# Kernel tuning notes

Hardware: AMD Instinct MI355X
Metric: run time of the kernel (lower is better)

Reference implementation:

```python
import jax, jax.numpy as jnp
import numpy as np
from jax import lax

B, CM, CQ, CO, H, W, KS = 8, 64, 64, 64, 128, 128, 3
K = KS * KS  # 9 kernel taps, offset_group=1


def setup_inputs() -> dict:
    key = jax.random.key(0)
    k1, k2, k3, k4 = jax.random.split(key, 4)
    mem = jax.random.normal(k1, (B, CM, H, W), jnp.float32)
    que = jax.random.normal(k2, (B, CQ, H, W), jnp.float32)
    # conv_offset: Conv2d(CM+CQ -> 3*K, 3x3, pad=1, bias=True); small init so offsets are a few px
    w_off = jax.random.normal(k3, (3 * K, CM + CQ, KS, KS), jnp.float32) * 0.01
    b_off = jnp.zeros((3 * K,), jnp.float32)
    # deformable conv weight: [CO, CM, 3, 3], bias=False
    w_def = jax.random.normal(k4, (CO, CM, KS, KS), jnp.float32) * (1.0 / np.sqrt(CM * K))
    return {"mem": mem, "que": que, "w_off": w_off, "b_off": b_off, "w_def": w_def}


def _deform_conv2d(mem, offset, mask, w_def):
    """Deformable conv v2 (stride=1, pad=1, dil=1, groups=1, offset_group=1).
    mem: [B,C,H,W]; offset: [B,2K,H,W] (dy,dx pairs per tap); mask: [B,K,H,W]."""
    Bn, C, Hn, Wn = mem.shape
    Kn = w_def.shape[2] * w_def.shape[3]
    off = offset.reshape(Bn, Kn, 2, Hn, Wn)
    dy, dx = off[:, :, 0], off[:, :, 1]            # [B,K,H,W]
    kk = jnp.arange(Kn)
    ky = (kk // KS - 1).astype(jnp.float32)        # kernel tap offsets with pad=1, dil=1
    kx = (kk % KS - 1).astype(jnp.float32)
    gy = jnp.arange(Hn, dtype=jnp.float32)
    gx = jnp.arange(Wn, dtype=jnp.float32)
    py = gy[None, None, :, None] + ky[None, :, None, None] + dy   # sample y coords [B,K,H,W]
    px = gx[None, None, None, :] + kx[None, :, None, None] + dx   # sample x coords [B,K,H,W]
    y0 = jnp.floor(py)
    x0 = jnp.floor(px)
    fy = py - y0
    fx = px - x0
    b_idx = jnp.arange(Bn)[:, None, None, None]

    def corner(iy, ix, wgt):
        valid = (iy >= 0) & (iy < Hn) & (ix >= 0) & (ix < Wn)  # zero padding outside
        iyc = jnp.clip(iy.astype(jnp.int32), 0, Hn - 1)
        ixc = jnp.clip(ix.astype(jnp.int32), 0, Wn - 1)
        vals = mem[b_idx, :, iyc, ixc]             # gather -> [B,K,H,W,C]
        return vals * (wgt * valid)[..., None]

    sampled = (corner(y0, x0, (1 - fy) * (1 - fx))
               + corner(y0, x0 + 1, (1 - fy) * fx)
               + corner(y0 + 1, x0, fy * (1 - fx))
               + corner(y0 + 1, x0 + 1, fy * fx))
    sampled = sampled * mask[..., None]            # modulation (applied raw, as in source)
    w = w_def.reshape(w_def.shape[0], C, Kn)       # [O,C,K]; tap order kh*KS+kw matches kk
    return jnp.einsum('bkhwc,ock->bohw', sampled, w)


def reference(mem, que, w_off, b_off, w_def):
    x = jnp.concatenate([mem, que], axis=1)
    off = lax.conv_general_dilated(
        x, w_off, window_strides=(1, 1), padding=[(1, 1), (1, 1)],
        dimension_numbers=('NCHW', 'OIHW', 'NCHW')) + b_off[None, :, None, None]
    offset, mask = off[:, :2 * K], off[:, 2 * K:]
    return _deform_conv2d(mem, offset, mask, w_def)
```

## Files before the change

kernel.cpp:

```cpp
#include <hip/hip_runtime.h>
#include <hip/hip_fp16.h>

#define Bn   8
#define CM_  64
#define CIN  128
#define CO_  64
#define Hn   128
#define Wn   128
#define Kn   9
#define COFF 27
#define HW   (Hn * Wn)

typedef __attribute__((ext_vector_type(8))) _Float16 f16x8;
typedef __attribute__((ext_vector_type(4))) float f32x4;

__device__ __forceinline__ unsigned h22u(__half2 h) {
    unsigned u; __builtin_memcpy(&u, &h, 4); return u;
}
__device__ __forceinline__ __half2 u2h2(unsigned u) {
    __half2 h; __builtin_memcpy(&h, &u, 4); return h;
}
__device__ __forceinline__ unsigned short f2h(float x) {
    __half h = __float2half(x);
    unsigned short u; __builtin_memcpy(&u, &h, 2); return u;
}

__global__ __launch_bounds__(256) void transpose_kernel(
    const float* __restrict__ mem, const float* __restrict__ que,
    uint4* __restrict__ xT4)
{
    __shared__ unsigned tile[64 * 65];

    const int bb   = blockIdx.x & 7;
    const int pix0 = (blockIdx.x >> 3) * 64;
    const int tid  = threadIdx.x;
    const int pxL  = tid & 63;
    const int cg   = tid >> 6;

    const float* mb = mem + (size_t)bb * CM_ * HW + pix0 + pxL;
    const float* qb = que + (size_t)bb * CM_ * HW + pix0 + pxL;

    #pragma unroll
    for (int i = 0; i < 16; ++i) {
        const int c = cg * 32 + 2 * i;
        const float v0 = (c < CM_) ? mb[(size_t)c * HW]       : qb[(size_t)(c - CM_) * HW];
        const float v1 = (c + 1 < CM_) ? mb[(size_t)(c + 1) * HW] : qb[(size_t)(c + 1 - CM_) * HW];
        tile[pxL * 65 + cg * 16 + i] = h22u(__floats2half2_rn(v0, v1));
    }
    __syncthreads();

    uint4* dst = xT4 + (size_t)(bb * HW + pix0) * 16;
    #pragma unroll
    for (int p = 0; p < 4; ++p) {
        const int G  = p * 256 + tid;
        const int px = G >> 4;
        const int u  = G & 15;
        uint4 v;
        v.x = tile[px * 65 + u * 4 + 0];
        v.y = tile[px * 65 + u * 4 + 1];
        v.z = tile[px * 65 + u * 4 + 2];
        v.w = tile[px * 65 + u * 4 + 3];
        dst[G] = v;
    }
}

__global__ __launch_bounds__(256) void wprep_all_kernel(
    const float* __restrict__ w_def, const float* __restrict__ w_off,
    unsigned short* __restrict__ wpd, unsigned short* __restrict__ wpo)
{
    int idx = blockIdx.x * 256 + threadIdx.x;
    if (idx < CO_ * CM_ * Kn) {
        const int j  = idx & 7;
        const int L  = (idx >> 3) & 63;
        const int f  = (idx >> 9) & 1;
        const int gk = idx >> 10;
        const int k  = gk % 9;
        const int g  = gk / 9;
        const int o  = g * 16 + (L & 15);
        const int c  = f * 32 + (L >> 4) * 8 + j;
        wpd[idx] = f2h(w_def[(size_t)(o * CM_ + c) * Kn + k]);
        return;
    }
    idx -= CO_ * CM_ * Kn;
    if (idx < 2 * 9 * 4 * 64 * 8) {
        const int j   = idx & 7;
        const int L   = (idx >> 3) & 63;
        const int s   = (idx >> 9) & 3;
        const int r   = idx >> 11;
        const int tap = r % 9;
        const int ot  = r / 9;
        const int o   = ot * 16 + (L & 15);
        const int c   = s * 32 + (L >> 4) * 8 + j;
        wpo[idx] = (o < COFF) ? f2h(w_off[(size_t)(o * CIN + c) * Kn + tap])
                              : (unsigned short)0;
    }
}

__global__ __launch_bounds__(256, 6) void fused_deform_kernel(
    const uint4* __restrict__ xT4, const uint4* __restrict__ wpo,
    const uint4* __restrict__ wpd, const float* __restrict__ b_off,
    float* __restrict__ out)
{
    __shared__ __align__(16) char lds[198 * 8 * 16];
    uint4* xw   = (uint4*)lds;
    float* offl = (float*)lds;
    uint4* smp4 = (uint4*)(lds + 8192);

    const int bb   = blockIdx.x & 7;
    const int pix0 = (blockIdx.x >> 3) * 64;
    const int h0   = pix0 >> 7;
    const int w0   = pix0 & 127;
    const int tid  = threadIdx.x;
    const int wv   = tid >> 6;
    const int lane = tid & 63;
    const int quad = lane >> 4;
    const int lrow = lane & 15;

    const uint4* xb = xT4 + (size_t)bb * HW * 16;

    {
        const int ot   = wv >> 1;
        const int sub0 = (wv & 1) * 2;

        f32x4 oacc[2];
        #pragma unroll
        for (int t = 0; t < 2; ++t)
            #pragma unroll
            for (int r = 0; r < 4; ++r) {
                const int o = ot * 16 + quad * 4 + r;
                oacc[t][r] = (o < COFF) ? b_off[o] : 0.0f;
            }

        #pragma unroll
        for (int Hh = 0; Hh < 2; ++Hh) {
            #pragma unroll
            for (int g = 0; g < 7; ++g) {
                const int idx = g * 256 + tid;
                if (idx < 198 * 8) {
                    const int slot = idx >> 3;
                    const int j    = idx & 7;
                    const int r    = slot / 66;
                    const int c    = slot - r * 66;
                    const int y    = h0 + r - 1;
                    const int x    = w0 + c - 1;
                    const bool ok  = (y >= 0) & (y < Hn) & (x >= 0) & (x < Wn);
                    uint4 v = make_uint4(0, 0, 0, 0);
                    if (ok) v = xb[(size_t)(y * Wn + x) * 16 + Hh * 8 + j];
                    xw[slot * 8 + (j ^ (slot & 7))] = v;
                }
            }
            __syncthreads();

            #pragma unroll
            for (int tap = 0; tap < 9; ++tap) {
                const int rr = tap / 3;
                const int cc = tap % 3;

                const uint4* ap = wpo
                    + (size_t)((ot * 9 + tap) * 4 + Hh * 2) * 64 + lane;
                f16x8 a[2];
                #pragma unroll
                for (int s = 0; s < 2; ++s)
                    a[s] = __builtin_bit_cast(f16x8, ap[s * 64]);

                #pragma unroll
                for (int t = 0; t < 2; ++t) {
                    const int pl   = (sub0 + t) * 16 + lrow;
                    const int slot = rr * 66 + pl + cc;
                    const int base = slot * 8;
                    const int sw   = slot & 7;
                    #pragma unroll
                    for (int s = 0; s < 2; ++s) {
                        const f16x8 bfrag = __builtin_bit_cast(f16x8,
                            xw[base + ((s * 4 + quad) ^ sw)]);
                        oacc[t] = __builtin_amdgcn_mfma_f32_16x16x32_f16(
                            a[s], bfrag, oacc[t], 0, 0, 0);
                    }
                }
            }
            __syncthreads();
        }

        #pragma unroll
        for (int t = 0; t < 2; ++t) {
            const int pl = (sub0 + t) * 16 + lrow;
            #pragma unroll
            for (int r = 0; r < 4; ++r) {
                const int o = ot * 16 + quad * 4 + r;
                if (o < COFF) offl[o * 64 + pl] = oacc[t][r];
            }
        }
        __syncthreads();
    }

    const int chunk = lane & 7;
    const int psub  = lane >> 3;

    const int pM = pix0 + lane;
    const int hM = pM >> 7;
    const int wM = pM & 127;

    f32x4 acc[4];
    #pragma unroll
    for (int i = 0; i < 4; ++i) acc[i] = (f32x4){0.f, 0.f, 0.f, 0.f};

    __half2 W00h[2], W01h[2], W10h[2], W11h[2];
    uint4   G00[2], G01[2], G10[2], G11[2];

    auto prep = [&](int k) {
        const float dy = offl[(2 * k    ) * 64 + lane];
        const float dx = offl[(2 * k + 1) * 64 + lane];
        const float mk = offl[(18 + k   ) * 64 + lane];
        const float py = (float)(hM + k / 3 - 1) + dy;
        const float px = (float)(wM + k % 3 - 1) + dx;
        const float y0f = floorf(py), x0f = floorf(px);
        const float fy = py - y0f,  fx = px - x0f;
        const int y0 = (int)y0f, x0 = (int)x0f;
        const int y1 = y0 + 1,   x1 = x0 + 1;
        const bool vy0 = (y0 >= 0) & (y0 < Hn);
        const bool vy1 = (y1 >= 0) & (y1 < Hn);
        const bool vx0 = (x0 >= 0) & (x0 < Wn);
        const bool vx1 = (x1 >= 0) & (x1 < Wn);
        const float w00 = (1.f - fy) * (1.f - fx) * (float)(vy0 & vx0) * mk;
        const float w01 = (1.f - fy) * fx         * (float)(vy0 & vx1) * mk;
        const float w10 = fy * (1.f - fx)         * (float)(vy1 & vx0) * mk;
        const float w11 = fy * fx                 * (float)(vy1 & vx1) * mk;
        const int y0c = min(max(y0, 0), Hn - 1);
        const int y1c = min(max(y1, 0), Hn - 1);
        const int x0c = min(max(x0, 0), Wn - 1);
        const int x1c = min(max(x1, 0), Wn - 1);
        const int i00 = y0c * Wn + x0c, i01 = y0c * Wn + x1c;
        const int i10 = y1c * Wn + x0c, i11 = y1c * Wn + x1c;

        #pragma unroll
        for (int g = 0; g < 2; ++g) {
            const int pl = g * 32 + wv * 8 + psub;
            W00h[g] = __float2half2_rn(__shfl(w00, pl, 64));
            W01h[g] = __float2half2_rn(__shfl(w01, pl, 64));
            W10h[g] = __float2half2_rn(__shfl(w10, pl, 64));
            W11h[g] = __float2half2_rn(__shfl(w11, pl, 64));
            const int I00 = __shfl(i00, pl, 64);
            const int I01 = __shfl(i01, pl, 64);
            const int I10 = __shfl(i10, pl, 64);
            const int I11 = __shfl(i11, pl, 64);
            G00[g] = xb[(size_t)I00 * 16 + chunk];
            G01[g] = xb[(size_t)I01 * 16 + chunk];
            G10[g] = xb[(size_t)I10 * 16 + chunk];
            G11[g] = xb[(size_t)I11 * 16 + chunk];
        }
    };

    auto blendwrite = [&](int buf) {
        #pragma unroll
        for (int g = 0; g < 2; ++g) {
            const int pl = g * 32 + wv * 8 + psub;
            const unsigned u00[4] = {G00[g].x, G00[g].y, G00[g].z, G00[g].w};
            const unsigned u01[4] = {G01[g].x, G01[g].y, G01[g].z, G01[g].w};
            const unsigned u10[4] = {G10[g].x, G10[g].y, G10[g].z, G10[g].w};
            const unsigned u11[4] = {G11[g].x, G11[g].y, G11[g].z, G11[g].w};
            unsigned pk[4];
            #pragma unroll
            for (int d = 0; d < 4; ++d) {
                __half2 s = __hmul2(u2h2(u00[d]), W00h[g]);
                s = __hfma2(u2h2(u01[d]), W01h[g], s);
                s = __hfma2(u2h2(u10[d]), W10h[g], s);
                s = __hfma2(u2h2(u11[d]), W11h[g], s);
                pk[d] = h22u(s);
            }
            smp4[buf * 512 + pl * 8 + (chunk ^ (pl & 7))] =
                make_uint4(pk[0], pk[1], pk[2], pk[3]);
        }
    };

    prep(0);
    blendwrite(0);
    __syncthreads();

    #pragma unroll
    for (int k = 0; k < Kn; ++k) {
        const int cur = k & 1;

        if (k < Kn - 1) prep(k + 1);

        const uint4* wpk = wpd + (size_t)((wv * 9 + k) * 2) * 64 + lane;
        const f16x8 a0 = __builtin_bit_cast(f16x8, wpk[0]);
        const f16x8 a1 = __builtin_bit_cast(f16x8, wpk[64]);

        #pragma unroll
        for (int nt = 0; nt < 4; ++nt) {
            const int pm = nt * 16 + lrow;
            const f16x8 b0 = __builtin_bit_cast(f16x8,
                smp4[cur * 512 + pm * 8 + ( quad      ^ (pm & 7))]);
            const f16x8 b1 = __builtin_bit_cast(f16x8,
                smp4[cur * 512 + pm * 8 + ((quad + 4) ^ (pm & 7))]);
            acc[nt] = __builtin_amdgcn_mfma_f32_16x16x32_f16(a0, b0, acc[nt], 0, 0, 0);
            acc[nt] = __builtin_amdgcn_mfma_f32_16x16x32_f16(a1, b1, acc[nt], 0, 0, 0);
        }

        if (k < Kn - 1) blendwrite(cur ^ 1);
        __syncthreads();
    }

    const int obase = (wv << 4) + (quad << 2);
    #pragma unroll
    for (int nt = 0; nt < 4; ++nt) {
        const int pp = pix0 + nt * 16 + lrow;
        #pragma unroll
        for (int r = 0; r < 4; ++r)
            out[(size_t)(bb * CO_ + obase + r) * HW + pp] = acc[nt][r];
    }
}

extern "C" void kernel_launch(void* const* d_in, const int* in_sizes, int n_in,
                              void* d_out, int out_size, void* d_ws, size_t ws_size,
                              hipStream_t stream) {
    const float* mem   = (const float*)d_in[0];
    const float* que   = (const float*)d_in[1];
    const float* w_off = (const float*)d_in[2];
    const float* b_off = (const float*)d_in[3];
    const float* w_def = (const float*)d_in[4];
    float* out = (float*)d_out;

    char* ws = (char*)d_ws;
    unsigned short* wpd = (unsigned short*)ws;
    unsigned short* wpo = (unsigned short*)(ws + 73728);
    uint4*          xT4 = (uint4*)(ws + 147456);

    transpose_kernel<<<2048, 256, 0, stream>>>(mem, que, xT4);
    wprep_all_kernel<<<288, 256, 0, stream>>>(w_def, w_off, wpd, wpo);
    fused_deform_kernel<<<2048, 256, 0, stream>>>(
        xT4, (const uint4*)wpo, (const uint4*)wpd, b_off, out);
}
```

Baseline: 180.3 us.

## Make deformable-conv phase wave-local to remove per-tap block barriers

Restructures the sampling/GEMM phase so each wave owns 16 pixels and computes all 64 output channels for them, instead of each wave owning 16 output channels across all 64 pixels. Each lane now computes its own bilinear weights and gathers, with no cross-lane shuffles. The sampled tile lives in a per-wave LDS region, which removes the per-tap __syncthreads. The weight-prep layout is reordered to match, the LDS layout is rearranged, one barrier in the offset-conv loop is skipped, and the occupancy hint in launch_bounds is dropped. In exchange, each wave loads all of the deform weights from global/cache every tap, and the per-wave LDS buffer relies on wave-synchronous ordering without an explicit barrier.

```diff
diff --git a/kernel.cpp b/kernel.cpp
--- a/kernel.cpp
+++ b/kernel.cpp
@@ -73,9 +73,9 @@
         const int j  = idx & 7;
         const int L  = (idx >> 3) & 63;
         const int f  = (idx >> 9) & 1;
-        const int gk = idx >> 10;
-        const int k  = gk % 9;
-        const int g  = gk / 9;
+        const int q  = idx >> 10;
+        const int k  = q >> 2;
+        const int g  = q & 3;
         const int o  = g * 16 + (L & 15);
         const int c  = f * 32 + (L >> 4) * 8 + j;
         wpd[idx] = f2h(w_def[(size_t)(o * CM_ + c) * Kn + k]);
@@ -96,15 +96,14 @@
     }
 }
 
-__global__ __launch_bounds__(256, 6) void fused_deform_kernel(
+__global__ __launch_bounds__(256) void fused_deform_kernel(
     const uint4* __restrict__ xT4, const uint4* __restrict__ wpo,
     const uint4* __restrict__ wpd, const float* __restrict__ b_off,
     float* __restrict__ out)
 {
-    __shared__ __align__(16) char lds[198 * 8 * 16];
+    __shared__ __align__(16) char lds[32256];
     uint4* xw   = (uint4*)lds;
-    float* offl = (float*)lds;
-    uint4* smp4 = (uint4*)(lds + 8192);
+    float* offl = (float*)(lds + 25344);
 
     const int bb   = blockIdx.x & 7;
     const int pix0 = (blockIdx.x >> 3) * 64;
@@ -178,7 +177,7 @@
                     }
                 }
             }
-            __syncthreads();
+            if (Hh == 0) __syncthreads();
         }
 
         #pragma unroll
@@ -193,28 +192,30 @@
         __syncthreads();
     }
 
-    const int chunk = lane & 7;
-    const int psub  = lane >> 3;
-
-    const int pM = pix0 + lane;
+    const int px = lane & 15;
+    const int cs = lane >> 4;
+    const int sp = wv * 16 + px;
+    const int pM = pix0 + sp;
     const int hM = pM >> 7;
     const int wM = pM & 127;
 
+    uint4* smpW = (uint4*)lds + wv * 256;
+
     f32x4 acc[4];
     #pragma unroll
     for (int i = 0; i < 4; ++i) acc[i] = (f32x4){0.f, 0.f, 0.f, 0.f};
 
-    __half2 W00h[2], W01h[2], W10h[2], W11h[2];
-    uint4   G00[2], G01[2], G10[2], G11[2];
+    __half2 Wc00, Wc01, Wc10, Wc11;
+    uint4 G[8];
 
     auto prep = [&](int k) {
-        const float dy = offl[(2 * k    ) * 64 + lane];
-        const float dx = offl[(2 * k + 1) * 64 + lane];
-        const float mk = offl[(18 + k   ) * 64 + lane];
-        const float py = (float)(hM + k / 3 - 1) + dy;
-        const float px = (float)(wM + k % 3 - 1) + dx;
-        const float y0f = floorf(py), x0f = floorf(px);
-        const float fy = py - y0f,  fx = px - x0f;
+        const float dy = offl[(2 * k    ) * 64 + sp];
+        const float dx = offl[(2 * k + 1) * 64 + sp];
+        const float mk = offl[(18 + k   ) * 64 + sp];
+        const float py  = (float)(hM + k / 3 - 1) + dy;
+        const float pxf = (float)(wM + k % 3 - 1) + dx;
+        const float y0f = floorf(py), x0f = floorf(pxf);
+        const float fy = py - y0f,  fx = pxf - x0f;
         const int y0 = (int)y0f, x0 = (int)x0f;
         const int y1 = y0 + 1,   x1 = x0 + 1;
         const bool vy0 = (y0 >= 0) & (y0 < Hn);
@@ -225,89 +226,76 @@
         const float w01 = (1.f - fy) * fx         * (float)(vy0 & vx1) * mk;
         const float w10 = fy * (1.f - fx)         * (float)(vy1 & vx0) * mk;
         const float w11 = fy * fx                 * (float)(vy1 & vx1) * mk;
+        Wc00 = __float2half2_rn(w00);
+        Wc01 = __float2half2_rn(w01);
+        Wc10 = __float2half2_rn(w10);
+        Wc11 = __float2half2_rn(w11);
         const int y0c = min(max(y0, 0), Hn - 1);
         const int y1c = min(max(y1, 0), Hn - 1);
         const int x0c = min(max(x0, 0), Wn - 1);
         const int x1c = min(max(x1, 0), Wn - 1);
         const int i00 = y0c * Wn + x0c, i01 = y0c * Wn + x1c;
         const int i10 = y1c * Wn + x0c, i11 = y1c * Wn + x1c;
-
-        #pragma unroll
-        for (int g = 0; g < 2; ++g) {
-            const int pl = g * 32 + wv * 8 + psub;
-            W00h[g] = __float2half2_rn(__shfl(w00, pl, 64));
-            W01h[g] = __float2half2_rn(__shfl(w01, pl, 64));
-            W10h[g] = __float2half2_rn(__shfl(w10, pl, 64));
-            W11h[g] = __float2half2_rn(__shfl(w11, pl, 64));
-            const int I00 = __shfl(i00, pl, 64);
-            const int I01 = __shfl(i01, pl, 64);
-            const int I10 = __shfl(i10, pl, 64);
-            const int I11 = __shfl(i11, pl, 64);
-            G00[g] = xb[(size_t)I00 * 16 + chunk];
-            G01[g] = xb[(size_t)I01 * 16 + chunk];
-            G10[g] = xb[(size_t)I10 * 16 + chunk];
-            G11[g] = xb[(size_t)I11 * 16 + chunk];
-        }
+        const uint4* p00 = xb + (size_t)i00 * 16 + cs;
+        const uint4* p01 = xb + (size_t)i01 * 16 + cs;
+        const uint4* p10 = xb + (size_t)i10 * 16 + cs;
+        const uint4* p11 = xb + (size_t)i11 * 16 + cs;
+        G[0] = p00[0]; G[1] = p00[4];
+        G[2] = p01[0]; G[3] = p01[4];
+        G[4] = p10[0]; G[5] = p10[4];
+        G[6] = p11[0]; G[7] = p11[4];
     };
 
-    auto blendwrite = [&](int buf) {
-        #pragma unroll
-        for (int g = 0; g < 2; ++g) {
-            const int pl = g * 32 + wv * 8 + psub;
-            const unsigned u00[4] = {G00[g].x, G00[g].y, G00[g].z, G00[g].w};
-            const unsigned u01[4] = {G01[g].x, G01[g].y, G01[g].z, G01[g].w};
-            const unsigned u10[4] = {G10[g].x, G10[g].y, G10[g].z, G10[g].w};
-            const unsigned u11[4] = {G11[g].x, G11[g].y, G11[g].z, G11[g].w};
+    auto blend_store = [&](int buf) {
+        #pragma unroll
+        for (int hh = 0; hh < 2; ++hh) {
+            const uint4 g00 = G[0 + hh], g01 = G[2 + hh];
+            const uint4 g10 = G[4 + hh], g11 = G[6 + hh];
+            const unsigned u00[4] = {g00.x, g00.y, g00.z, g00.w};
+            const unsigned u01[4] = {g01.x, g01.y, g01.z, g01.w};
+            const unsigned u10[4] = {g10.x, g10.y, g10.z, g10.w};
+            const unsigned u11[4] = {g11.x, g11.y, g11.z, g11.w};
             unsigned pk[4];
             #pragma unroll
             for (int d = 0; d < 4; ++d) {
-                __half2 s = __hmul2(u2h2(u00[d]), W00h[g]);
-                s = __hfma2(u2h2(u01[d]), W01h[g], s);
-                s = __hfma2(u2h2(u10[d]), W10h[g], s);
-                s = __hfma2(u2h2(u11[d]), W11h[g], s);
+                __half2 s = __hmul2(u2h2(u00[d]), Wc00);
+                s = __hfma2(u2h2(u01[d]), Wc01, s);
+                s = __hfma2(u2h2(u10[d]), Wc10, s);
+                s = __hfma2(u2h2(u11[d]), Wc11, s);
                 pk[d] = h22u(s);
             }
-            smp4[buf * 512 + pl * 8 + (chunk ^ (pl & 7))] =
+            smpW[buf * 128 + px * 8 + ((cs + hh * 4) ^ (px & 7))] =
                 make_uint4(pk[0], pk[1], pk[2], pk[3]);
         }
     };
 
     prep(0);
-    blendwrite(0);
-    __syncthreads();
-
     #pragma unroll
     for (int k = 0; k < Kn; ++k) {
-        const int cur = k & 1;
-
+        const int buf = k & 1;
+        blend_store(buf);
         if (k < Kn - 1) prep(k + 1);
 
-        const uint4* wpk = wpd + (size_t)((wv * 9 + k) * 2) * 64 + lane;
-        const f16x8 a0 = __builtin_bit_cast(f16x8, wpk[0]);
-        const f16x8 a1 = __builtin_bit_cast(f16x8, wpk[64]);
-
-        #pragma unroll
-        for (int nt = 0; nt < 4; ++nt) {
-            const int pm = nt * 16 + lrow;
-            const f16x8 b0 = __builtin_bit_cast(f16x8,
-                smp4[cur * 512 + pm * 8 + ( quad      ^ (pm & 7))]);
-            const f16x8 b1 = __builtin_bit_cast(f16x8,
-                smp4[cur * 512 + pm * 8 + ((quad + 4) ^ (pm & 7))]);
-            acc[nt] = __builtin_amdgcn_mfma_f32_16x16x32_f16(a0, b0, acc[nt], 0, 0, 0);
-            acc[nt] = __builtin_amdgcn_mfma_f32_16x16x32_f16(a1, b1, acc[nt], 0, 0, 0);
+        const f16x8 b0 = __builtin_bit_cast(f16x8,
+            smpW[buf * 128 + px * 8 + ( cs      ^ (px & 7))]);
+        const f16x8 b1 = __builtin_bit_cast(f16x8,
+            smpW[buf * 128 + px * 8 + ((cs + 4) ^ (px & 7))]);
+
+        #pragma unroll
+        for (int g = 0; g < 4; ++g) {
+            const uint4* wpk = wpd + (size_t)((k * 4 + g) * 2) * 64 + lane;
+            const f16x8 a0 = __builtin_bit_cast(f16x8, wpk[0]);
+            const f16x8 a1 = __builtin_bit_cast(f16x8, wpk[64]);
+            acc[g] = __builtin_amdgcn_mfma_f32_16x16x32_f16(a0, b0, acc[g], 0, 0, 0);
+            acc[g] = __builtin_amdgcn_mfma_f32_16x16x32_f16(a1, b1, acc[g], 0, 0, 0);
         }
-
-        if (k < Kn - 1) blendwrite(cur ^ 1);
-        __syncthreads();
-    }
-
-    const int obase = (wv << 4) + (quad << 2);
-    #pragma unroll
-    for (int nt = 0; nt < 4; ++nt) {
-        const int pp = pix0 + nt * 16 + lrow;
+    }
+
+    #pragma unroll
+    for (int g = 0; g < 4; ++g) {
         #pragma unroll
         for (int r = 0; r < 4; ++r)
-            out[(size_t)(bb * CO_ + obase + r) * HW + pp] = acc[nt][r];
+            out[(size_t)(bb * CO_ + g * 16 + cs * 4 + r) * HW + pM] = acc[g][r];
     }
 }
 
```

Result: slower. 210.7 us (+16.9%).
